# Kernel optimization log

Measured on AMD Instinct MI355X. Metric: run time of the kernel, lower is better.

The kernel has to match this reference:

```python
import jax, jax.numpy as jnp
import numpy as np

N_NODES = 50000
N_EDGES = 800000
DIM = 128
LN_EPS = 1e-5


def setup_inputs() -> dict:
    key = jax.random.key(0)
    k1, k2, k3, k4, k5 = jax.random.split(key, 5)
    x = jax.random.normal(k1, (N_NODES, DIM), dtype=jnp.float32)
    edge_index = jax.random.randint(k2, (2, N_EDGES), 0, N_NODES, dtype=jnp.int64)
    edge_weight = jax.random.uniform(k3, (N_EDGES,), dtype=jnp.float32)
    # GCNConv linear (PyG Linear: out = x @ W.T + b)
    W = jax.random.normal(k4, (DIM, DIM), dtype=jnp.float32) / np.sqrt(DIM)
    b = jnp.zeros((DIM,), dtype=jnp.float32)
    # pygnn.LayerNorm(dim, mode='node') affine params
    ln_weight = jnp.ones((DIM,), dtype=jnp.float32)
    ln_bias = jnp.zeros((DIM,), dtype=jnp.float32)
    return {"x": x, "edge_index": edge_index, "edge_weight": edge_weight,
            "W": W, "b": b, "ln_weight": ln_weight, "ln_bias": ln_bias}


def reference(x, edge_index, edge_weight, W, b, ln_weight, ln_bias):
    n = x.shape[0]
    # --- LayerNorm (mode='node'): per-node over feature dim ---
    mu = jnp.mean(x, axis=-1, keepdims=True)
    var = jnp.mean(jnp.square(x - mu), axis=-1, keepdims=True)
    xn = (x - mu) * jax.lax.rsqrt(var + LN_EPS) * ln_weight + ln_bias
    # --- GCNConv: linear first, then normalized propagate ---
    h = xn @ W.T  # [N, dim]
    row, col = edge_index[0], edge_index[1]  # source, target
    # add self loops (fill_value = 1.0)
    loop = jnp.arange(n, dtype=edge_index.dtype)
    row_f = jnp.concatenate([row, loop])
    col_f = jnp.concatenate([col, loop])
    ew_f = jnp.concatenate([edge_weight, jnp.ones((n,), dtype=edge_weight.dtype)])
    # symmetric gcn normalization: deg over target (col)
    deg = jax.ops.segment_sum(ew_f, col_f, num_segments=n)
    dinv = jnp.where(deg > 0, jax.lax.rsqrt(deg), 0.0)
    norm = dinv[row_f] * ew_f * dinv[col_f]  # [E+N]
    # gather-scale-scatter
    msg = h[row_f] * norm[:, None]  # [E+N, dim]
    out = jax.ops.segment_sum(msg, col_f, num_segments=n) + b
    # --- GELU (torch default = exact erf form); dropout is identity (p=0 / eval) ---
    return jax.nn.gelu(out, approximate=False)
```

## Files before the change

### kernel.cpp

```cpp
#include <hip/hip_runtime.h>
#include <math.h>

#define DIM 128
#define LN_EPS 1e-5f

typedef __attribute__((ext_vector_type(8))) short short8;
typedef __attribute__((ext_vector_type(4))) float floatx4;

__device__ __forceinline__ float gelu_exact(float v) {
    return 0.5f * v * (1.0f + erff(v * 0.70710678118654752f));
}
__device__ __forceinline__ float bf2f(unsigned short u) {
    return __uint_as_float(((unsigned)u) << 16);
}
__device__ __forceinline__ short f2bf(float f) {
    unsigned b = __float_as_uint(f);
    return (short)((b + 0x7FFF + ((b >> 16) & 1)) >> 16);
}

__global__ __launch_bounds__(256) void gemm_rank_kernel(
    const float* __restrict__ x, const float* __restrict__ W,
    const float* __restrict__ lnw, const float* __restrict__ lnb,
    unsigned short* __restrict__ h16,
    const int* __restrict__ col, int* __restrict__ cnt, int* __restrict__ rnk,
    int n, int E)
{
    const int tid = threadIdx.x;

    if ((int)(blockIdx.x % 3) == 2) {
        int rb   = blockIdx.x / 3;
        int base = rb * 2048 + tid;
        #pragma unroll
        for (int it = 0; it < 8; ++it) {
            int e = base + it * 256;
            if (e < E) rnk[e] = atomicAdd(&cnt[col[e]], 1);
        }
        return;
    }

    __shared__ short swb[2048 * 8];
    __shared__ short axb[1024 * 8];

    const int gb = blockIdx.x - (blockIdx.x + 1) / 3;
    const int n0 = gb * 64;

    for (int c = tid; c < 2048; c += 256) {
        int nrow = ((c >> 8) << 4) | (c & 15);
        int kb   = (((c >> 6) & 3) << 5) + (((c >> 4) & 3) << 3);
        const float* wp = W + nrow * DIM + kb;
        float4 w0 = *(const float4*)wp;
        float4 w1 = *(const float4*)(wp + 4);
        short8 p;
        p[0] = f2bf(w0.x); p[1] = f2bf(w0.y); p[2] = f2bf(w0.z); p[3] = f2bf(w0.w);
        p[4] = f2bf(w1.x); p[5] = f2bf(w1.y); p[6] = f2bf(w1.z); p[7] = f2bf(w1.w);
        *(short8*)&swb[c * 8] = p;
    }

    {
        int m = tid >> 2, sub = tid & 3;
        int node = n0 + m;
        bool valid = (node < n);
        const float4* xp = (const float4*)(x + (size_t)node * DIM + sub * 32);
        float4 v[8];
        float s = 0.f, ss = 0.f;
        #pragma unroll
        for (int i = 0; i < 8; ++i) {
            v[i] = valid ? xp[i] : make_float4(0.f, 0.f, 0.f, 0.f);
            s  += v[i].x + v[i].y + v[i].z + v[i].w;
            ss += v[i].x * v[i].x + v[i].y * v[i].y + v[i].z * v[i].z + v[i].w * v[i].w;
        }
        s += __shfl_xor(s, 1); ss += __shfl_xor(ss, 1);
        s += __shfl_xor(s, 2); ss += __shfl_xor(ss, 2);
        float mu   = s * (1.0f / 128.0f);
        float var  = ss * (1.0f / 128.0f) - mu * mu;
        float rstd = rsqrtf(var + LN_EPS);

        int mt = m >> 4, mloc = m & 15;
        #pragma unroll
        for (int quad = 0; quad < 4; ++quad) {
            float4 a = v[2 * quad], c4 = v[2 * quad + 1];
            const float4* lw = (const float4*)(lnw + sub * 32 + quad * 8);
            const float4* lb = (const float4*)(lnb + sub * 32 + quad * 8);
            float4 lw0 = lw[0], lw1 = lw[1], lb0 = lb[0], lb1 = lb[1];
            short8 p;
            p[0] = f2bf((a.x  - mu) * rstd * lw0.x + lb0.x);
            p[1] = f2bf((a.y  - mu) * rstd * lw0.y + lb0.y);
            p[2] = f2bf((a.z  - mu) * rstd * lw0.z + lb0.z);
            p[3] = f2bf((a.w  - mu) * rstd * lw0.w + lb0.w);
            p[4] = f2bf((c4.x - mu) * rstd * lw1.x + lb1.x);
            p[5] = f2bf((c4.y - mu) * rstd * lw1.y + lb1.y);
            p[6] = f2bf((c4.z - mu) * rstd * lw1.z + lb1.z);
            p[7] = f2bf((c4.w - mu) * rstd * lw1.w + lb1.w);
            int slot = mt * 256 + sub * 64 + quad * 16 + mloc;
            *(short8*)&axb[slot * 8] = p;
        }
    }
    __syncthreads();

    const int w    = tid >> 6;
    const int lane = tid & 63;

    short8 afrag[4];
    #pragma unroll
    for (int kq = 0; kq < 4; ++kq)
        afrag[kq] = *(const short8*)&axb[(w * 256 + kq * 64 + lane) * 8];

    floatx4 acc[8];
    #pragma unroll
    for (int jt = 0; jt < 8; ++jt) acc[jt] = (floatx4){0.f, 0.f, 0.f, 0.f};

    #pragma unroll
    for (int jt = 0; jt < 8; ++jt) {
        #pragma unroll
        for (int kq = 0; kq < 4; ++kq) {
            short8 bfrag = *(const short8*)&swb[(jt * 256 + kq * 64 + lane) * 8];
            acc[jt] = __builtin_amdgcn_mfma_f32_16x16x32_bf16(afrag[kq], bfrag,
                                                              acc[jt], 0, 0, 0);
        }
    }

    const int quad = lane >> 4, nl = lane & 15;
    #pragma unroll
    for (int jt = 0; jt < 8; ++jt) {
        #pragma unroll
        for (int r = 0; r < 4; ++r) {
            int rnode = n0 + w * 16 + quad * 4 + r;
            if (rnode < n)
                h16[(size_t)rnode * DIM + jt * 16 + nl] = (unsigned short)f2bf(acc[jt][r]);
        }
    }
}

__global__ __launch_bounds__(256) void scan_a_kernel(
    const int* __restrict__ cnt, int* __restrict__ bsum, int n)
{
    __shared__ int lds[256];
    int t = threadIdx.x, b = blockIdx.x;
    int base = b * 1024 + t * 4;
    int s = 0;
    if (base + 3 < n) {
        int4 c4 = *(const int4*)(cnt + base);
        s = c4.x + c4.y + c4.z + c4.w;
    } else {
        for (int i = 0; i < 4; ++i) if (base + i < n) s += cnt[base + i];
    }
    lds[t] = s; __syncthreads();
    for (int off = 128; off > 0; off >>= 1) {
        if (t < off) lds[t] += lds[t + off];
        __syncthreads();
    }
    if (t == 0) bsum[b] = lds[0];
}

__global__ __launch_bounds__(256) void scan_bc_kernel(
    const int* __restrict__ cnt, const int* __restrict__ bsum,
    int* __restrict__ offsets, int nb, int n)
{
    __shared__ int lds[256];
    int t = threadIdx.x, b = blockIdx.x;
    int pre0 = 0, total = 0;
    for (int i = 0; i < nb; ++i) {
        int v = bsum[i];
        if (i < b) pre0 += v;
        total += v;
    }
    int base = b * 1024 + t * 4;
    int v0 = 0, v1 = 0, v2 = 0, v3 = 0;
    bool full = (base + 3 < n);
    if (full) {
        int4 c4 = *(const int4*)(cnt + base);
        v0 = c4.x; v1 = c4.y; v2 = c4.z; v3 = c4.w;
    } else {
        if (base     < n) v0 = cnt[base];
        if (base + 1 < n) v1 = cnt[base + 1];
        if (base + 2 < n) v2 = cnt[base + 2];
        if (base + 3 < n) v3 = cnt[base + 3];
    }
    int s = v0 + v1 + v2 + v3;
    lds[t] = s; __syncthreads();
    int inc = s;
    for (int off = 1; off < 256; off <<= 1) {
        int add = (t >= off) ? lds[t - off] : 0;
        __syncthreads();
        inc += add;
        lds[t] = inc;
        __syncthreads();
    }
    int pre = pre0 + inc - s;
    int o0 = pre, o1 = pre + v0, o2 = o1 + v1, o3 = o2 + v2;
    if (full) {
        *(int4*)(offsets + base) = make_int4(o0, o1, o2, o3);
    } else {
        int oo[4] = {o0, o1, o2, o3};
        for (int i = 0; i < 4; ++i) if (base + i < n) offsets[base + i] = oo[i];
    }
    if (b == 0 && t == 0) offsets[n] = total;
}

__global__ __launch_bounds__(256) void scatter_fill_kernel(
    const int* __restrict__ row, const int* __restrict__ col,
    const float* __restrict__ ew, const int* __restrict__ rank,
    const int* __restrict__ offsets, int2* __restrict__ edge_s, int E)
{
    int e = blockIdx.x * 256 + threadIdx.x;
    if (e < E) {
        int c = col[e];
        int pos = offsets[c] + rank[e];
        edge_s[pos] = make_int2(row[e], __float_as_int(ew[e]));
    }
}

__global__ __launch_bounds__(256) void deg_dinv_kernel(
    const int* __restrict__ offsets, const int2* __restrict__ edge_s,
    float* __restrict__ dinv, int n)
{
    int i = blockIdx.x * 256 + threadIdx.x;
    if (i < n) {
        int beg = offsets[i], end = offsets[i + 1];
        float s = 1.0f;
        for (int j = beg; j < end; ++j) s += __int_as_float(edge_s[j].y);
        dinv[i] = rsqrtf(s);
    }
}

__global__ __launch_bounds__(256) void gather4_kernel(
    const int* __restrict__ offsets, const int2* __restrict__ edge_s,
    const float* __restrict__ dinv, const unsigned short* __restrict__ h16,
    const float* __restrict__ bias, float* __restrict__ out, int n)
{
    int wave = (blockIdx.x * 256 + threadIdx.x) >> 6;
    int lane = threadIdx.x & 63;
    int grp  = lane >> 4;
    int sub  = lane & 15;
    int node = wave * 4 + grp;
    if (node >= n) return;

    int beg = offsets[node], end = offsets[node + 1];
    float di = dinv[node];
    short8 sv = *(const short8*)(h16 + (size_t)node * DIM + sub * 8);
    float s2 = di * di;
    float acc[8];
    #pragma unroll
    for (int d = 0; d < 8; ++d) acc[d] = s2 * bf2f((unsigned short)sv[d]);

    int j = beg;
    for (; j + 1 < end; j += 2) {
        int2 e0 = edge_s[j], e1 = edge_s[j + 1];
        float n0 = dinv[e0.x] * __int_as_float(e0.y) * di;
        float n1 = dinv[e1.x] * __int_as_float(e1.y) * di;
        short8 a = *(const short8*)(h16 + (size_t)e0.x * DIM + sub * 8);
        short8 c = *(const short8*)(h16 + (size_t)e1.x * DIM + sub * 8);
        #pragma unroll
        for (int d = 0; d < 8; ++d) acc[d] = fmaf(n0, bf2f((unsigned short)a[d]), acc[d]);
        #pragma unroll
        for (int d = 0; d < 8; ++d) acc[d] = fmaf(n1, bf2f((unsigned short)c[d]), acc[d]);
    }
    if (j < end) {
        int2 e0 = edge_s[j];
        float n0 = dinv[e0.x] * __int_as_float(e0.y) * di;
        short8 a = *(const short8*)(h16 + (size_t)e0.x * DIM + sub * 8);
        #pragma unroll
        for (int d = 0; d < 8; ++d) acc[d] = fmaf(n0, bf2f((unsigned short)a[d]), acc[d]);
    }

    float4 b0 = *(const float4*)(bias + sub * 8);
    float4 b1 = *(const float4*)(bias + sub * 8 + 4);
    float4 o0, o1;
    o0.x = gelu_exact(acc[0] + b0.x); o0.y = gelu_exact(acc[1] + b0.y);
    o0.z = gelu_exact(acc[2] + b0.z); o0.w = gelu_exact(acc[3] + b0.w);
    o1.x = gelu_exact(acc[4] + b1.x); o1.y = gelu_exact(acc[5] + b1.y);
    o1.z = gelu_exact(acc[6] + b1.z); o1.w = gelu_exact(acc[7] + b1.w);
    float* op = out + (size_t)node * DIM + sub * 8;
    *(float4*)op       = o0;
    *(float4*)(op + 4) = o1;
}

extern "C" void kernel_launch(void* const* d_in, const int* in_sizes, int n_in,
                              void* d_out, int out_size, void* d_ws, size_t ws_size,
                              hipStream_t stream)
{
    const float* x    = (const float*)d_in[0];
    const int*   ei   = (const int*)d_in[1];
    const float* ew   = (const float*)d_in[2];
    const float* W    = (const float*)d_in[3];
    const float* b    = (const float*)d_in[4];
    const float* ln_w = (const float*)d_in[5];
    const float* ln_b = (const float*)d_in[6];
    float* out = (float*)d_out;

    const int n = in_sizes[0] / DIM;
    const int E = in_sizes[2];
    const int* row  = ei;
    const int* colp = ei + E;

    const int NB = (n + 1023) / 1024;

    int2*           edge_s  = (int2*)d_ws;
    unsigned short* h16     = (unsigned short*)(edge_s + E);
    int*            cnt     = (int*)(h16 + (size_t)n * DIM);
    int*            rank    = cnt + n;
    int*            offsets = rank + E;
    int*            bsum    = offsets + n + 1;
    float*          dinv    = (float*)(bsum + 4096);

    const int GB = (n + 63) / 64;
    const int RB = (E + 2047) / 2048;
    int T = GB + RB;
    while (T / 3 < RB || T - T / 3 < GB) ++T;

    hipMemsetAsync(cnt, 0, (size_t)n * sizeof(int), stream);
    gemm_rank_kernel<<<T, 256, 0, stream>>>(x, W, ln_w, ln_b, h16,
                                            colp, cnt, rank, n, E);
    scan_a_kernel<<<NB, 256, 0, stream>>>(cnt, bsum, n);
    scan_bc_kernel<<<NB, 256, 0, stream>>>(cnt, bsum, offsets, NB, n);
    scatter_fill_kernel<<<(E + 255) / 256, 256, 0, stream>>>(row, colp, ew, rank,
                                                             offsets, edge_s, E);
    deg_dinv_kernel<<<(n + 255) / 256, 256, 0, stream>>>(offsets, edge_s, dinv, n);
    {
        int waves = (n + 3) / 4;
        int blocks = (waves + 3) / 4;
        gather4_kernel<<<blocks, 256, 0, stream>>>(offsets, edge_s, dinv, h16, b, out, n);
    }
}
```

Before: 191.4 us.

## Pack count and degree into double atomics, precompute edge norms in scatter

The rank pass now does one double-precision atomic per edge that adds 2^32 plus the edge weight, so a single atomic yields both the rank and the weighted degree. The accumulators are split into 8 replicas to reduce contention, and the scan emits offsets per replica and computes dinv directly. This removes the separate degree kernel. The scatter stores the fully normalized edge weight, so the gather no longer does a random dinv lookup, and its loop is unrolled to 4 edges. In exchange, fp64 atomics and 8x larger accumulator and offset arrays add memset and scan traffic. The exactness of the degree sum depends on double precision.

Measured after the change: 193.8 us. No clear change (+1.2%).

```diff
diff --git a/kernel.cpp b/kernel.cpp
--- a/kernel.cpp
+++ b/kernel.cpp
@@ -3,6 +3,8 @@
 
 #define DIM 128
 #define LN_EPS 1e-5f
+#define TWO32 4294967296.0
+#define INV32 (1.0 / 4294967296.0)
 
 typedef __attribute__((ext_vector_type(8))) short short8;
 typedef __attribute__((ext_vector_type(4))) float floatx4;
@@ -22,18 +24,26 @@
     const float* __restrict__ x, const float* __restrict__ W,
     const float* __restrict__ lnw, const float* __restrict__ lnb,
     unsigned short* __restrict__ h16,
-    const int* __restrict__ col, int* __restrict__ cnt, int* __restrict__ rnk,
+    const int* __restrict__ col, const float* __restrict__ ew,
+    double* __restrict__ acc8, int* __restrict__ rnk,
     int n, int E)
 {
     const int tid = threadIdx.x;
 
     if ((int)(blockIdx.x % 3) == 2) {
         int rb   = blockIdx.x / 3;
+        int r    = rb & 7;
+        size_t rbase = (size_t)r * n;
         int base = rb * 2048 + tid;
         #pragma unroll
         for (int it = 0; it < 8; ++it) {
             int e = base + it * 256;
-            if (e < E) rnk[e] = atomicAdd(&cnt[col[e]], 1);
+            if (e < E) {
+                int c = col[e];
+                double old = atomicAdd(&acc8[rbase + c], TWO32 + (double)ew[e]);
+                int rk = (int)(old * INV32);
+                rnk[e] = (r << 24) | rk;
+            }
         }
         return;
     }
@@ -132,17 +142,21 @@
 }
 
 __global__ __launch_bounds__(256) void scan_a_kernel(
-    const int* __restrict__ cnt, int* __restrict__ bsum, int n)
+    const double* __restrict__ acc8, int* __restrict__ bsum, int n)
 {
     __shared__ int lds[256];
     int t = threadIdx.x, b = blockIdx.x;
     int base = b * 1024 + t * 4;
     int s = 0;
-    if (base + 3 < n) {
-        int4 c4 = *(const int4*)(cnt + base);
-        s = c4.x + c4.y + c4.z + c4.w;
-    } else {
-        for (int i = 0; i < 4; ++i) if (base + i < n) s += cnt[base + i];
+    #pragma unroll
+    for (int i = 0; i < 4; ++i) {
+        int c = base + i;
+        if (c < n) {
+            int k = 0;
+            for (int r = 0; r < 8; ++r)
+                k += (int)(acc8[(size_t)r * n + c] * INV32);
+            s += k;
+        }
     }
     lds[t] = s; __syncthreads();
     for (int off = 128; off > 0; off >>= 1) {
@@ -153,8 +167,8 @@
 }
 
 __global__ __launch_bounds__(256) void scan_bc_kernel(
-    const int* __restrict__ cnt, const int* __restrict__ bsum,
-    int* __restrict__ offsets, int nb, int n)
+    const double* __restrict__ acc8, const int* __restrict__ bsum,
+    int* __restrict__ off8, float* __restrict__ dinv, int nb, int n)
 {
     __shared__ int lds[256];
     int t = threadIdx.x, b = blockIdx.x;
@@ -165,18 +179,25 @@
         total += v;
     }
     int base = b * 1024 + t * 4;
-    int v0 = 0, v1 = 0, v2 = 0, v3 = 0;
-    bool full = (base + 3 < n);
-    if (full) {
-        int4 c4 = *(const int4*)(cnt + base);
-        v0 = c4.x; v1 = c4.y; v2 = c4.z; v3 = c4.w;
-    } else {
-        if (base     < n) v0 = cnt[base];
-        if (base + 1 < n) v1 = cnt[base + 1];
-        if (base + 2 < n) v2 = cnt[base + 2];
-        if (base + 3 < n) v3 = cnt[base + 3];
-    }
-    int s = v0 + v1 + v2 + v3;
+
+    int k8[4][8];
+    int ksum[4];
+    double wsum[4];
+    #pragma unroll
+    for (int i = 0; i < 4; ++i) {
+        ksum[i] = 0; wsum[i] = 0.0;
+        int c = base + i;
+        if (c < n) {
+            for (int r = 0; r < 8; ++r) {
+                double v = acc8[(size_t)r * n + c];
+                int k = (int)(v * INV32);
+                k8[i][r] = k;
+                ksum[i] += k;
+                wsum[i] += v - (double)k * TWO32;
+            }
+        }
+    }
+    int s = ksum[0] + ksum[1] + ksum[2] + ksum[3];
     lds[t] = s; __syncthreads();
     int inc = s;
     for (int off = 1; off < 256; off <<= 1) {
@@ -187,39 +208,38 @@
         __syncthreads();
     }
     int pre = pre0 + inc - s;
-    int o0 = pre, o1 = pre + v0, o2 = o1 + v1, o3 = o2 + v2;
-    if (full) {
-        *(int4*)(offsets + base) = make_int4(o0, o1, o2, o3);
-    } else {
-        int oo[4] = {o0, o1, o2, o3};
-        for (int i = 0; i < 4; ++i) if (base + i < n) offsets[base + i] = oo[i];
-    }
-    if (b == 0 && t == 0) offsets[n] = total;
+    #pragma unroll
+    for (int i = 0; i < 4; ++i) {
+        int c = base + i;
+        if (c < n) {
+            int run = pre;
+            for (int r = 0; r < 8; ++r) {
+                off8[(size_t)r * (n + 1) + c] = run;
+                run += k8[i][r];
+            }
+            dinv[c] = rsqrtf(1.0f + (float)wsum[i]);
+            pre = run;
+        }
+    }
+    if (b == 0 && t == 0) off8[n] = total;
 }
 
 __global__ __launch_bounds__(256) void scatter_fill_kernel(
     const int* __restrict__ row, const int* __restrict__ col,
-    const float* __restrict__ ew, const int* __restrict__ rank,
-    const int* __restrict__ offsets, int2* __restrict__ edge_s, int E)
+    const float* __restrict__ ew, const int* __restrict__ rnk,
+    const int* __restrict__ off8, const float* __restrict__ dinv,
+    int2* __restrict__ edge_s, int n, int E)
 {
     int e = blockIdx.x * 256 + threadIdx.x;
     if (e < E) {
-        int c = col[e];
-        int pos = offsets[c] + rank[e];
-        edge_s[pos] = make_int2(row[e], __float_as_int(ew[e]));
-    }
-}
-
-__global__ __launch_bounds__(256) void deg_dinv_kernel(
-    const int* __restrict__ offsets, const int2* __restrict__ edge_s,
-    float* __restrict__ dinv, int n)
-{
-    int i = blockIdx.x * 256 + threadIdx.x;
-    if (i < n) {
-        int beg = offsets[i], end = offsets[i + 1];
-        float s = 1.0f;
-        for (int j = beg; j < end; ++j) s += __int_as_float(edge_s[j].y);
-        dinv[i] = rsqrtf(s);
+        int c  = col[e];
+        int pk = rnk[e];
+        int r  = pk >> 24;
+        int rk = pk & 0xFFFFFF;
+        int pos = off8[(size_t)r * (n + 1) + c] + rk;
+        int src = row[e];
+        float nr = dinv[src] * ew[e] * dinv[c];
+        edge_s[pos] = make_int2(src, __float_as_int(nr));
     }
 }
 
@@ -244,20 +264,26 @@
     for (int d = 0; d < 8; ++d) acc[d] = s2 * bf2f((unsigned short)sv[d]);
 
     int j = beg;
-    for (; j + 1 < end; j += 2) {
-        int2 e0 = edge_s[j], e1 = edge_s[j + 1];
-        float n0 = dinv[e0.x] * __int_as_float(e0.y) * di;
-        float n1 = dinv[e1.x] * __int_as_float(e1.y) * di;
-        short8 a = *(const short8*)(h16 + (size_t)e0.x * DIM + sub * 8);
-        short8 c = *(const short8*)(h16 + (size_t)e1.x * DIM + sub * 8);
-        #pragma unroll
-        for (int d = 0; d < 8; ++d) acc[d] = fmaf(n0, bf2f((unsigned short)a[d]), acc[d]);
-        #pragma unroll
-        for (int d = 0; d < 8; ++d) acc[d] = fmaf(n1, bf2f((unsigned short)c[d]), acc[d]);
-    }
-    if (j < end) {
+    for (; j + 3 < end; j += 4) {
+        int2 e0 = edge_s[j],     e1 = edge_s[j + 1];
+        int2 e2 = edge_s[j + 2], e3 = edge_s[j + 3];
+        short8 a0 = *(const short8*)(h16 + (size_t)e0.x * DIM + sub * 8);
+        short8 a1 = *(const short8*)(h16 + (size_t)e1.x * DIM + sub * 8);
+        short8 a2 = *(const short8*)(h16 + (size_t)e2.x * DIM + sub * 8);
+        short8 a3 = *(const short8*)(h16 + (size_t)e3.x * DIM + sub * 8);
+        float n0 = __int_as_float(e0.y), n1 = __int_as_float(e1.y);
+        float n2 = __int_as_float(e2.y), n3 = __int_as_float(e3.y);
+        #pragma unroll
+        for (int d = 0; d < 8; ++d) {
+            acc[d] = fmaf(n0, bf2f((unsigned short)a0[d]), acc[d]);
+            acc[d] = fmaf(n1, bf2f((unsigned short)a1[d]), acc[d]);
+            acc[d] = fmaf(n2, bf2f((unsigned short)a2[d]), acc[d]);
+            acc[d] = fmaf(n3, bf2f((unsigned short)a3[d]), acc[d]);
+        }
+    }
+    for (; j < end; ++j) {
         int2 e0 = edge_s[j];
-        float n0 = dinv[e0.x] * __int_as_float(e0.y) * di;
+        float n0 = __int_as_float(e0.y);
         short8 a = *(const short8*)(h16 + (size_t)e0.x * DIM + sub * 8);
         #pragma unroll
         for (int d = 0; d < 8; ++d) acc[d] = fmaf(n0, bf2f((unsigned short)a[d]), acc[d]);
@@ -295,12 +321,12 @@
 
     const int NB = (n + 1023) / 1024;
 
-    int2*           edge_s  = (int2*)d_ws;
+    double*         acc8    = (double*)d_ws;
+    int2*           edge_s  = (int2*)(acc8 + (size_t)8 * n);
     unsigned short* h16     = (unsigned short*)(edge_s + E);
-    int*            cnt     = (int*)(h16 + (size_t)n * DIM);
-    int*            rank    = cnt + n;
-    int*            offsets = rank + E;
-    int*            bsum    = offsets + n + 1;
+    int*            rnk     = (int*)(h16 + (size_t)n * DIM);
+    int*            off8    = rnk + E;
+    int*            bsum    = off8 + (size_t)8 * (n + 1);
     float*          dinv    = (float*)(bsum + 4096);
 
     const int GB = (n + 63) / 64;
@@ -308,17 +334,16 @@
     int T = GB + RB;
     while (T / 3 < RB || T - T / 3 < GB) ++T;
 
-    hipMemsetAsync(cnt, 0, (size_t)n * sizeof(int), stream);
+    hipMemsetAsync(acc8, 0, (size_t)8 * n * sizeof(double), stream);
     gemm_rank_kernel<<<T, 256, 0, stream>>>(x, W, ln_w, ln_b, h16,
-                                            colp, cnt, rank, n, E);
-    scan_a_kernel<<<NB, 256, 0, stream>>>(cnt, bsum, n);
-    scan_bc_kernel<<<NB, 256, 0, stream>>>(cnt, bsum, offsets, NB, n);
-    scatter_fill_kernel<<<(E + 255) / 256, 256, 0, stream>>>(row, colp, ew, rank,
-                                                             offsets, edge_s, E);
-    deg_dinv_kernel<<<(n + 255) / 256, 256, 0, stream>>>(offsets, edge_s, dinv, n);
+                                            colp, ew, acc8, rnk, n, E);
+    scan_a_kernel<<<NB, 256, 0, stream>>>(acc8, bsum, n);
+    scan_bc_kernel<<<NB, 256, 0, stream>>>(acc8, bsum, off8, dinv, NB, n);
+    scatter_fill_kernel<<<(E + 255) / 256, 256, 0, stream>>>(row, colp, ew, rnk,
+                                                             off8, dinv, edge_s, n, E);
     {
-        int waves = (n + 3) / 4;
+        int waves  = (n + 3) / 4;
         int blocks = (waves + 3) / 4;
-        gather4_kernel<<<blocks, 256, 0, stream>>>(offsets, edge_s, dinv, h16, b, out, n);
-    }
-}
+        gather4_kernel<<<blocks, 256, 0, stream>>>(off8, edge_s, dinv, h16, b, out, n);
+    }
+}
```
